# Kernel optimization log

Measured on AMD Instinct MI355X. Metric: run time of the kernel, lower is better.

The kernel has to match this reference:

```python
import jax, jax.numpy as jnp
import numpy as np
from jax import lax

# dims
B, T, D = 2, 1024, 512
H, K, V = 8, 64, 64      # head_k_dim = head_v_dim = 64
CONV = 4
# IVON / module hyperparams (from __init__ defaults)
LR, B1, B2, WD, LAM = 1e-3, 0.9, 0.999, 0.0, 1.0
EPS = 1e-5               # RMSNorm eps
SCALE = K ** -0.5


def _silu(x):
    return x * jax.nn.sigmoid(x)


def _short_conv(x, w):
    """Causal depthwise conv1d (kernel_size=CONV, no bias) + SiLU. x:[B,T,C], w:[C,CONV]."""
    xp = jnp.pad(x, ((0, 0), (CONV - 1, 0), (0, 0)))
    y = sum(xp[:, i:i + x.shape[1]] * w[:, i] for i in range(CONV))
    return _silu(y)


def _l2norm(x):
    return x * lax.rsqrt(jnp.sum(x * x, -1, keepdims=True) + 1e-6)


def setup_inputs() -> dict:
    key = jax.random.key(0)
    ks = jax.random.split(key, 10)
    s = 0.02
    return {
        "hidden_states": jax.random.normal(ks[0], (B, T, D), jnp.float32),
        "Wq": jax.random.normal(ks[1], (D, H * K), jnp.float32) * s,
        "Wk": jax.random.normal(ks[2], (D, H * K), jnp.float32) * s,
        "Wv": jax.random.normal(ks[3], (D, H * V), jnp.float32) * s,
        "Wb": jax.random.normal(ks[4], (D, H), jnp.float32) * s,
        "cw_q": jax.random.normal(ks[5], (H * K, CONV), jnp.float32) * 0.5,
        "cw_k": jax.random.normal(ks[6], (H * K, CONV), jnp.float32) * 0.5,
        "cw_v": jax.random.normal(ks[7], (H * V, CONV), jnp.float32) * 0.5,
        "rms_w": jnp.ones((V,), jnp.float32),
        "Wo": jax.random.normal(ks[8], (H * V, D), jnp.float32) * s,
    }


def reference(hidden_states, Wq, Wk, Wv, Wb, cw_q, cw_k, cw_v, rms_w, Wo):
    x = hidden_states
    # projections -> causal depthwise short conv (+SiLU, qk_activation='silu')
    q = _short_conv(x @ Wq, cw_q).reshape(B, T, H, K)
    k = _short_conv(x @ Wk, cw_k).reshape(B, T, H, K)
    v = _short_conv(x @ Wv, cw_v).reshape(B, T, H, V)
    beta = jax.nn.sigmoid(x @ Wb)                     # [B,T,H]
    # qk l2-norm inside kernel (qk_norm='l2'), scale on q
    q = _l2norm(q) * SCALE
    k = _l2norm(k)

    # fused recurrent IVON delta-rule: per-step outer-product gradient of
    # 0.5||k @ S - v||^2, momentum g, diag preconditioner h (noise-free IVON).
    def step(carry, inp):
        S, h, g = carry                               # each [B,H,K,V]
        qt, kt, vt, bt = inp                          # [B,H,K],[B,H,K],[B,H,V],[B,H]
        pred = jnp.einsum('bhk,bhkv->bhv', kt, S)
        grad = kt[..., None] * (pred - vt)[..., None, :]   # [B,H,K,V]
        g = B1 * g + (1.0 - B1) * grad
        h = B2 * h + (1.0 - B2) * grad * grad
        S = S - LR * bt[..., None, None] * (g + WD * S) / (h + LAM)
        o = jnp.einsum('bhk,bhkv->bhv', qt, S)
        return (S, h, g), o

    z = jnp.zeros((B, H, K, V), jnp.float32)
    inps = (jnp.swapaxes(q, 0, 1), jnp.swapaxes(k, 0, 1),
            jnp.swapaxes(v, 0, 1), jnp.swapaxes(beta, 0, 1))
    _, o = lax.scan(step, (z, z, z), inps)            # o: [T,B,H,V]
    o = jnp.swapaxes(o, 0, 1)                          # [B,T,H,V]

    # RMSNorm over head_v_dim, then output projection
    o = o * lax.rsqrt(jnp.mean(o * o, -1, keepdims=True) + EPS) * rms_w
    o = o.reshape(B, T, H * V) @ Wo                    # [B,T,D]
    return o
```

## Files before the change

### kernel.cpp

```cpp
#include <hip/hip_runtime.h>
#include <hip/hip_bf16.h>
#include <math.h>

#define Bb 2
#define Tt 1024
#define Dd 512
#define Hh 8
#define Kk 64
#define Vv 64
#define BT (Bb*Tt)
#define HK (Hh*Kk)

#define B1c 0.9f
#define B2c 0.999f
#define LRc 1e-3f
#define SCALEc 0.125f

typedef short s8v __attribute__((ext_vector_type(8)));
typedef float f4v __attribute__((ext_vector_type(4)));

__device__ __forceinline__ unsigned short f2bf(float x) {
  unsigned u = __float_as_uint(x);
  u += 0x7FFFu + ((u >> 16) & 1u);
  return (unsigned short)(u >> 16);
}
__device__ __forceinline__ float bf2f(unsigned short h) {
  return __uint_as_float((unsigned)h << 16);
}

template <int CTRL>
__device__ __forceinline__ float dpp_add(float v) {
  int y = __builtin_amdgcn_update_dpp(0, __float_as_int(v), CTRL, 0xF, 0xF, true);
  return v + __int_as_float(y);
}

typedef unsigned uint2_t __attribute__((ext_vector_type(2)));

__device__ __forceinline__ float xor16_add(float x) {
#if __has_builtin(__builtin_amdgcn_permlane16_swap)
  uint2_t r = __builtin_amdgcn_permlane16_swap(__float_as_uint(x), __float_as_uint(x),
                                               false, false);
  return __uint_as_float(r.x) + __uint_as_float(r.y);
#else
  int y = __builtin_amdgcn_ds_swizzle(__float_as_int(x), 0x401F);
  return x + __int_as_float(y);
#endif
}

__device__ __forceinline__ float xor32_add(float x) {
#if __has_builtin(__builtin_amdgcn_permlane32_swap)
  uint2_t r = __builtin_amdgcn_permlane32_swap(__float_as_uint(x), __float_as_uint(x),
                                               false, false);
  return __uint_as_float(r.x) + __uint_as_float(r.y);
#else
  return x + __shfl_xor(x, 32, 64);
#endif
}

__device__ __forceinline__ float reduce16(float x) {
  x = dpp_add<0xB1>(x);
  x = dpp_add<0x4E>(x);
  x = dpp_add<0x141>(x);
  x = dpp_add<0x140>(x);
  return x;
}

__device__ __forceinline__ float reduce64(float x) {
  x = reduce16(x);
  x = xor16_add(x);
  x = xor32_add(x);
  return x;
}

__global__ __launch_bounds__(256) void cvt_x_kernel(
    const float* __restrict__ x, unsigned short* __restrict__ hi,
    unsigned short* __restrict__ lo) {
  const int i = (blockIdx.x * 256 + threadIdx.x) * 8;
  float4 a = *(const float4*)(x + i);
  float4 b = *(const float4*)(x + i + 4);
  const float v[8] = {a.x, a.y, a.z, a.w, b.x, b.y, b.z, b.w};
  union { unsigned short u[8]; uint4 q; } ph, pl;
#pragma unroll
  for (int j = 0; j < 8; ++j) {
    unsigned short h = f2bf(v[j]);
    ph.u[j] = h;
    pl.u[j] = f2bf(v[j] - bf2f(h));
  }
  *(uint4*)(hi + i) = ph.q;
  *(uint4*)(lo + i) = pl.q;
}

__global__ __launch_bounds__(256) void cvt_w_kernel(
    const float* __restrict__ W0, const float* __restrict__ W1,
    const float* __restrict__ W2,
    unsigned short* __restrict__ hib, unsigned short* __restrict__ lob) {
  __shared__ float Ts[64][65];
  const int z = blockIdx.z;
  const float* W = (z == 0) ? W0 : (z == 1) ? W1 : W2;
  unsigned short* hi = hib + (size_t)z * 512 * 512;
  unsigned short* lo = lob + (size_t)z * 512 * 512;
  const int tk = blockIdx.x * 64;
  const int tn = blockIdx.y * 64;
  const int r  = threadIdx.x >> 2;
  const int cg = threadIdx.x & 3;
#pragma unroll
  for (int j = 0; j < 4; ++j) {
    float4 v = *(const float4*)(W + (size_t)(tk + r) * 512 + tn + cg * 16 + j * 4);
    Ts[r][cg * 16 + j * 4 + 0] = v.x;
    Ts[r][cg * 16 + j * 4 + 1] = v.y;
    Ts[r][cg * 16 + j * 4 + 2] = v.z;
    Ts[r][cg * 16 + j * 4 + 3] = v.w;
  }
  __syncthreads();
  union { unsigned short u[16]; uint4 q[2]; } ph, pl;
#pragma unroll
  for (int j = 0; j < 16; ++j) {
    float v = Ts[cg * 16 + j][r];
    unsigned short h = f2bf(v);
    ph.u[j] = h;
    pl.u[j] = f2bf(v - bf2f(h));
  }
  const size_t ob = (size_t)(tn + r) * 512 + tk + cg * 16;
  *(uint4*)(hi + ob) = ph.q[0];
  *(uint4*)(hi + ob + 8) = ph.q[1];
  *(uint4*)(lo + ob) = pl.q[0];
  *(uint4*)(lo + ob + 8) = pl.q[1];
}

__device__ __forceinline__ void gemm_mfma_body(
    const unsigned short* __restrict__ Ahi, const unsigned short* __restrict__ Alo,
    const unsigned short* __restrict__ Bhi, const unsigned short* __restrict__ Blo,
    float* __restrict__ C) {
  __shared__ unsigned short Ah[64][40], Al[64][40], Bh[64][40], Bl[64][40];
  const int tid = threadIdx.x;
  const int bm = blockIdx.x * 64;
  const int bn = blockIdx.y * 64;
  const int srow = tid >> 2;
  const int skoff = (tid & 3) * 8;
  const int l = tid & 63, w = tid >> 6;
  const int arow = (l & 15) + 16 * w;
  const int koff = (l >> 4) * 8;

  const unsigned short* pAh = Ahi + (size_t)(bm + srow) * 512 + skoff;
  const unsigned short* pAl = Alo + (size_t)(bm + srow) * 512 + skoff;
  const unsigned short* pBh = Bhi + (size_t)(bn + srow) * 512 + skoff;
  const unsigned short* pBl = Blo + (size_t)(bn + srow) * 512 + skoff;

  f4v acc0 = {0.f, 0.f, 0.f, 0.f}, acc1 = acc0, acc2 = acc0, acc3 = acc0;

  uint4 rah = *(const uint4*)(pAh);
  uint4 ral = *(const uint4*)(pAl);
  uint4 rbh = *(const uint4*)(pBh);
  uint4 rbl = *(const uint4*)(pBl);

  for (int k0 = 0; k0 < 512; k0 += 32) {
    __syncthreads();
    *(uint4*)&Ah[srow][skoff] = rah;
    *(uint4*)&Al[srow][skoff] = ral;
    *(uint4*)&Bh[srow][skoff] = rbh;
    *(uint4*)&Bl[srow][skoff] = rbl;
    __syncthreads();
    if (k0 + 32 < 512) {
      rah = *(const uint4*)(pAh + k0 + 32);
      ral = *(const uint4*)(pAl + k0 + 32);
      rbh = *(const uint4*)(pBh + k0 + 32);
      rbl = *(const uint4*)(pBl + k0 + 32);
    }
    const s8v ah = *(const s8v*)&Ah[arow][koff];
    const s8v al = *(const s8v*)&Al[arow][koff];
#pragma unroll
    for (int c = 0; c < 4; ++c) {
      const s8v bh = *(const s8v*)&Bh[16 * c + (l & 15)][koff];
      const s8v bl = *(const s8v*)&Bl[16 * c + (l & 15)][koff];
      f4v* acc = (c == 0) ? &acc0 : (c == 1) ? &acc1 : (c == 2) ? &acc2 : &acc3;
      *acc = __builtin_amdgcn_mfma_f32_16x16x32_bf16(al, bh, *acc, 0, 0, 0);
      *acc = __builtin_amdgcn_mfma_f32_16x16x32_bf16(ah, bl, *acc, 0, 0, 0);
      *acc = __builtin_amdgcn_mfma_f32_16x16x32_bf16(ah, bh, *acc, 0, 0, 0);
    }
  }

  const int crow = bm + 16 * w + (l >> 4) * 4;
  const int ccol = bn + (l & 15);
#pragma unroll
  for (int i = 0; i < 4; ++i) {
    C[(size_t)(crow + i) * 512 + ccol + 0]  = acc0[i];
    C[(size_t)(crow + i) * 512 + ccol + 16] = acc1[i];
    C[(size_t)(crow + i) * 512 + ccol + 32] = acc2[i];
    C[(size_t)(crow + i) * 512 + ccol + 48] = acc3[i];
  }
}

__global__ __launch_bounds__(256) void gemm3_mfma_kernel(
    const unsigned short* __restrict__ xhi, const unsigned short* __restrict__ xlo,
    const unsigned short* __restrict__ whi, const unsigned short* __restrict__ wlo,
    float* __restrict__ qp, float* __restrict__ kp, float* __restrict__ vp) {
  const int z = blockIdx.z;
  float* Cp = (z == 0) ? qp : (z == 1) ? kp : vp;
  gemm_mfma_body(xhi, xlo, whi + (size_t)z * 512 * 512, wlo + (size_t)z * 512 * 512, Cp);
}

__global__ __launch_bounds__(256) void gemm1_mfma_kernel(
    const unsigned short* __restrict__ ahi, const unsigned short* __restrict__ alo,
    const unsigned short* __restrict__ whi, const unsigned short* __restrict__ wlo,
    float* __restrict__ C) {
  gemm_mfma_body(ahi, alo, whi, wlo, C);
}

__global__ __launch_bounds__(256) void beta_kernel(const float* __restrict__ x,
                                                   const float* __restrict__ Wb,
                                                   float* __restrict__ beta) {
  int gid = blockIdx.x * blockDim.x + threadIdx.x;
  int bt = gid >> 3, h = gid & 7;
  const float4* xr = (const float4*)(x + (size_t)bt * Dd);
  float s = 0.f;
#pragma unroll 4
  for (int d4 = 0; d4 < Dd / 4; ++d4) {
    float4 xv = xr[d4];
    const float* wb = Wb + (d4 * 4) * Hh + h;
    s = fmaf(xv.x, wb[0 * Hh], s);
    s = fmaf(xv.y, wb[1 * Hh], s);
    s = fmaf(xv.z, wb[2 * Hh], s);
    s = fmaf(xv.w, wb[3 * Hh], s);
  }
  beta[gid] = 1.f / (1.f + expf(-s));
}

__global__ __launch_bounds__(256) void conv_kernel(
    const float* __restrict__ qp, const float* __restrict__ kp,
    const float* __restrict__ vp,
    const float* __restrict__ cwq, const float* __restrict__ cwk,
    const float* __restrict__ cwv,
    float* __restrict__ qc, float* __restrict__ kc, float* __restrict__ vc) {
  const int mode = blockIdx.z;
  const float* pre; const float* cw; float* post;
  if (mode == 0)      { pre = qp; cw = cwq; post = qc; }
  else if (mode == 1) { pre = kp; cw = cwk; post = kc; }
  else                { pre = vp; cw = cwv; post = vc; }

  const int idx = blockIdx.x * 4 + (threadIdx.x >> 6);
  const int lane = threadIdx.x & 63;
  const int b = idx >> 13;
  const int th = idx & 8191;
  const int t = th >> 3;
  const int h = th & 7;
  const int ch = h * 64 + lane;

  float y = 0.f;
#pragma unroll
  for (int i = 0; i < 4; ++i) {
    int tt = t + i - 3;
    if (tt >= 0)
      y += pre[((size_t)(b * Tt + tt)) * HK + ch] * cw[ch * 4 + i];
  }
  y = y / (1.f + expf(-y));
  if (mode < 2) {
    float ss = reduce64(y * y);
    y *= rsqrtf(ss + 1e-6f);
    if (mode == 0) y *= SCALEc;
  }
  post[((size_t)(b * Tt + t)) * HK + ch] = y;
}

#define TC 32
#define NT (Tt / TC)

__global__ __launch_bounds__(512) void scan_kernel(
    const float* __restrict__ qc, const float* __restrict__ kc,
    const float* __restrict__ vc, const float* __restrict__ beta,
    float* __restrict__ o) {
  __shared__ float  ks[3][TC][64];
  __shared__ float  qs[3][TC][64];
  __shared__ float2 vb[3][TC][4];
  __shared__ float  Sb[2][TC][4][64];

  const int tid  = threadIdx.x;
  const int lane = tid & 63;
  const int wave = tid >> 6;
  const int bid  = blockIdx.x;
  const int vq   = bid >> 4;
  const int bh   = bid & 15;
  const int b = bh >> 3, h = bh & 7;

  const size_t base2 = ((size_t)b * Tt) * HK + h * 64;
  const float* bp = beta + ((size_t)b * Tt) * Hh + h;

  const int tid2 = tid - 256;
  const int sr = (tid2 & 255) >> 4;
  const int sg = tid2 & 15;
  const int vr = (tid2 & 255) >> 3;
  const int vcc = tid2 & 3;

  if (wave >= 4) {
    float4 k0 = *(const float4*)(kc + base2 + (size_t)sr * HK + sg * 4);
    float4 q0 = *(const float4*)(qc + base2 + (size_t)sr * HK + sg * 4);
    float4 k1 = *(const float4*)(kc + base2 + (size_t)(sr + 16) * HK + sg * 4);
    float4 q1 = *(const float4*)(qc + base2 + (size_t)(sr + 16) * HK + sg * 4);
    *(float4*)&ks[0][sr][sg * 4] = k0;
    *(float4*)&qs[0][sr][sg * 4] = q0;
    *(float4*)&ks[0][sr + 16][sg * 4] = k1;
    *(float4*)&qs[0][sr + 16][sg * 4] = q1;
    if ((tid2 & 7) < 4) {
      float vv = vc[base2 + (size_t)vr * HK + vq * 4 + vcc];
      float lb = (0.1f * LRc) * bp[(size_t)vr * Hh];
      vb[0][vr][vcc] = make_float2(vv, lb);
    }
  }
  __syncthreads();

  float S = 0.f, G = 0.f, H = 0.f, r = 1.f;
  float pred = 0.f;

  int d = 0;
  for (int tile = 0; tile < NT; ++tile) {
    const int dn = (d + 1 == 3) ? 0 : d + 1;
    const int dm = (d == 0) ? 2 : d - 1;
    const int sb = tile & 1, sbp = sb ^ 1;
    const int t0 = tile * TC;
    const int more = (tile + 1 < NT);

    if (wave < 4) {
      const int w = wave;
      pred = reduce64(ks[d][0][lane] * S);
#pragma unroll
      for (int s = 0; s < TC; ++s) {
        const float kv = ks[d][s][lane];
        const float2 vbc = vb[d][s][w];
        const float diff = pred - vbc.x;
        const float lrb = vbc.y;
        const float gr = kv * diff;
        G = fmaf(B1c, G, gr);
        H = fmaf(B2c, H, gr * gr);
        const float dd = fmaf(H, 0.001f, 1.0f);
        r = r * fmaf(-dd, r, 2.0f);
        S = fmaf(-lrb, G * r, S);
        Sb[sb][s][w][lane] = S;
        if (s + 1 < TC)
          pred = reduce64(ks[d][s + 1][lane] * S);
      }
    } else {
      float4 nk0, nq0, nk1, nq1; float nv = 0.f, nb = 0.f;
      if (more) {
        const int tn = t0 + TC;
        nk0 = *(const float4*)(kc + base2 + (size_t)(tn + sr) * HK + sg * 4);
        nq0 = *(const float4*)(qc + base2 + (size_t)(tn + sr) * HK + sg * 4);
        nk1 = *(const float4*)(kc + base2 + (size_t)(tn + sr + 16) * HK + sg * 4);
        nq1 = *(const float4*)(qc + base2 + (size_t)(tn + sr + 16) * HK + sg * 4);
        if ((tid2 & 7) < 4) {
          nv = vc[base2 + (size_t)(tn + vr) * HK + vq * 4 + vcc];
          nb = (0.1f * LRc) * bp[(size_t)(tn + vr) * Hh];
        }
      }
      if (tile > 0) {
        const int cb = wave - 4;
        float* opc = o + base2 + vq * 4 + cb;
        const int tp0 = t0 - TC;
#pragma unroll
        for (int s = 0; s < TC; ++s) {
          const float qv = qs[dm][s][lane];
          const float Sv = Sb[sbp][s][cb][lane];
          const float po = reduce64(qv * Sv);
          opc[(size_t)(tp0 + s) * HK] = po;
        }
      }
      if (more) {
        *(float4*)&ks[dn][sr][sg * 4] = nk0;
        *(float4*)&qs[dn][sr][sg * 4] = nq0;
        *(float4*)&ks[dn][sr + 16][sg * 4] = nk1;
        *(float4*)&qs[dn][sr + 16][sg * 4] = nq1;
        if ((tid2 & 7) < 4) vb[dn][vr][vcc] = make_float2(nv, nb);
      }
    }
    __syncthreads();
    d = dn;
  }

  if (wave >= 4) {
    const int dlast = (NT - 1) % 3;
    const int sbl = (NT - 1) & 1;
    const int cb = wave - 4;
    float* opc = o + base2 + vq * 4 + cb;
    const int tp0 = (NT - 1) * TC;
#pragma unroll
    for (int s = 0; s < TC; ++s) {
      const float qv = qs[dlast][s][lane];
      const float Sv = Sb[sbl][s][cb][lane];
      const float po = reduce64(qv * Sv);
      opc[(size_t)(tp0 + s) * HK] = po;
    }
  }
}

__global__ __launch_bounds__(256) void rmsnorm_kernel(
    const float* __restrict__ o, const float* __restrict__ rmsw,
    unsigned short* __restrict__ hi, unsigned short* __restrict__ lo) {
  const int idx = blockIdx.x * 4 + (threadIdx.x >> 6);
  const int lane = threadIdx.x & 63;
  const float* p = o + (size_t)idx * 64;
  float y = p[lane];
  float ss = reduce64(y * y);
  y = y * rsqrtf(ss * (1.f / 64.f) + 1e-5f) * rmsw[lane];
  unsigned short h = f2bf(y);
  hi[(size_t)idx * 64 + lane] = h;
  lo[(size_t)idx * 64 + lane] = f2bf(y - bf2f(h));
}

extern "C" void kernel_launch(void* const* d_in, const int* in_sizes, int n_in,
                              void* d_out, int out_size, void* d_ws, size_t ws_size,
                              hipStream_t stream) {
  const float* x    = (const float*)d_in[0];
  const float* Wq   = (const float*)d_in[1];
  const float* Wk   = (const float*)d_in[2];
  const float* Wv   = (const float*)d_in[3];
  const float* Wb   = (const float*)d_in[4];
  const float* cwq  = (const float*)d_in[5];
  const float* cwk  = (const float*)d_in[6];
  const float* cwv  = (const float*)d_in[7];
  const float* rmsw = (const float*)d_in[8];
  const float* Wo   = (const float*)d_in[9];
  float* out = (float*)d_out;
  float* ws  = (float*)d_ws;

  const size_t SZ = (size_t)BT * HK;
  float* qp   = ws;
  float* kp   = ws + 1 * SZ;
  float* vp   = ws + 2 * SZ;
  float* qc   = ws + 3 * SZ;
  float* kc   = ws + 4 * SZ;
  float* vc   = ws + 5 * SZ;
  float* beta = ws + 6 * SZ;
  float* on   = qp;

  unsigned short* xhi  = (unsigned short*)qc;
  unsigned short* xlo  = xhi + SZ;
  unsigned short* wh3  = (unsigned short*)kc;
  unsigned short* wl3  = wh3 + 3 * 512 * 512;
  unsigned short* wohi = (unsigned short*)vc;
  unsigned short* wolo = wohi + 512 * 512;
  unsigned short* onhi = (unsigned short*)kp;
  unsigned short* onlo = (unsigned short*)vp;

  cvt_x_kernel<<<dim3(BT * Dd / (256 * 8)), 256, 0, stream>>>(x, xhi, xlo);
  cvt_w_kernel<<<dim3(8, 8, 3), 256, 0, stream>>>(Wq, Wk, Wv, wh3, wl3);
  gemm3_mfma_kernel<<<dim3(BT / 64, HK / 64, 3), 256, 0, stream>>>(
      xhi, xlo, wh3, wl3, qp, kp, vp);
  beta_kernel<<<dim3(BT * Hh / 256), 256, 0, stream>>>(x, Wb, beta);
  conv_kernel<<<dim3(Bb * Tt * Hh / 4, 1, 3), 256, 0, stream>>>(
      qp, kp, vp, cwq, cwk, cwv, qc, kc, vc);
  scan_kernel<<<dim3(Bb * Hh * (Vv / 4)), 512, 0, stream>>>(
      qc, kc, vc, beta, on);
  cvt_w_kernel<<<dim3(8, 8, 1), 256, 0, stream>>>(Wo, Wo, Wo, wohi, wolo);
  rmsnorm_kernel<<<dim3(Bb * Tt * Hh / 4), 256, 0, stream>>>(on, rmsw, onhi, onlo);
  gemm1_mfma_kernel<<<dim3(BT / 64, HK / 64, 1), 256, 0, stream>>>(
      onhi, onlo, wohi, wolo, out);
}
```

Measured before the change: 180.4 us.

## Pack scan state into one compute wave with 4 K-rows per lane

The recurrent scan now runs in a single wave instead of four. Each lane holds four K entries of the state, and 16 lanes cover one V column, so each step's prediction needs a 16-lane reduction rather than a 64-lane one. The goal is to shorten the serial per-timestep reduction chain and add instruction-level parallelism on the critical path. The block shrinks to 320 threads, with four loader/output waves kept as before. The trade-off is more registers per lane and more per-step arithmetic serialized within that one wave.

```diff
diff --git a/kernel.cpp b/kernel.cpp
--- a/kernel.cpp
+++ b/kernel.cpp
@@ -264,7 +264,7 @@
 #define TC 32
 #define NT (Tt / TC)
 
-__global__ __launch_bounds__(512) void scan_kernel(
+__global__ __launch_bounds__(320) void scan_kernel(
     const float* __restrict__ qc, const float* __restrict__ kc,
     const float* __restrict__ vc, const float* __restrict__ beta,
     float* __restrict__ o) {
@@ -284,13 +284,16 @@
   const size_t base2 = ((size_t)b * Tt) * HK + h * 64;
   const float* bp = beta + ((size_t)b * Tt) * Hh + h;
 
-  const int tid2 = tid - 256;
+  const int g    = lane & 15;
+  const int cgrp = lane >> 4;
+
+  const int tid2 = tid - 64;
   const int sr = (tid2 & 255) >> 4;
   const int sg = tid2 & 15;
   const int vr = (tid2 & 255) >> 3;
   const int vcc = tid2 & 3;
 
-  if (wave >= 4) {
+  if (wave >= 1) {
     float4 k0 = *(const float4*)(kc + base2 + (size_t)sr * HK + sg * 4);
     float4 q0 = *(const float4*)(qc + base2 + (size_t)sr * HK + sg * 4);
     float4 k1 = *(const float4*)(kc + base2 + (size_t)(sr + 16) * HK + sg * 4);
@@ -307,8 +310,10 @@
   }
   __syncthreads();
 
-  float S = 0.f, G = 0.f, H = 0.f, r = 1.f;
-  float pred = 0.f;
+  float S0 = 0, S1 = 0, S2 = 0, S3 = 0;
+  float G0 = 0, G1 = 0, G2 = 0, G3 = 0;
+  float H0 = 0, H1 = 0, H2 = 0, H3 = 0;
+  float r0 = 1.f, r1 = 1.f, r2 = 1.f, r3 = 1.f;
 
   int d = 0;
   for (int tile = 0; tile < NT; ++tile) {
@@ -318,24 +323,46 @@
     const int t0 = tile * TC;
     const int more = (tile + 1 < NT);
 
-    if (wave < 4) {
-      const int w = wave;
-      pred = reduce64(ks[d][0][lane] * S);
+    if (wave == 0) {
+      float4 kt = *(const float4*)&ks[d][0][g * 4];
+      float pred = reduce16(fmaf(kt.x, S0, kt.y * S1) +
+                            fmaf(kt.z, S2, kt.w * S3));
 #pragma unroll
       for (int s = 0; s < TC; ++s) {
-        const float kv = ks[d][s][lane];
-        const float2 vbc = vb[d][s][w];
+        const float4 kv = *(const float4*)&ks[d][s][g * 4];
+        const float2 vbc = vb[d][s][cgrp];
         const float diff = pred - vbc.x;
         const float lrb = vbc.y;
-        const float gr = kv * diff;
-        G = fmaf(B1c, G, gr);
-        H = fmaf(B2c, H, gr * gr);
-        const float dd = fmaf(H, 0.001f, 1.0f);
-        r = r * fmaf(-dd, r, 2.0f);
-        S = fmaf(-lrb, G * r, S);
-        Sb[sb][s][w][lane] = S;
-        if (s + 1 < TC)
-          pred = reduce64(ks[d][s + 1][lane] * S);
+        const float gr0 = kv.x * diff;
+        const float gr1 = kv.y * diff;
+        const float gr2 = kv.z * diff;
+        const float gr3 = kv.w * diff;
+        G0 = fmaf(B1c, G0, gr0);
+        G1 = fmaf(B1c, G1, gr1);
+        G2 = fmaf(B1c, G2, gr2);
+        G3 = fmaf(B1c, G3, gr3);
+        H0 = fmaf(B2c, H0, gr0 * gr0);
+        H1 = fmaf(B2c, H1, gr1 * gr1);
+        H2 = fmaf(B2c, H2, gr2 * gr2);
+        H3 = fmaf(B2c, H3, gr3 * gr3);
+        const float d0 = fmaf(H0, 0.001f, 1.0f);
+        const float d1 = fmaf(H1, 0.001f, 1.0f);
+        const float d2 = fmaf(H2, 0.001f, 1.0f);
+        const float d3 = fmaf(H3, 0.001f, 1.0f);
+        r0 = r0 * fmaf(-d0, r0, 2.0f);
+        r1 = r1 * fmaf(-d1, r1, 2.0f);
+        r2 = r2 * fmaf(-d2, r2, 2.0f);
+        r3 = r3 * fmaf(-d3, r3, 2.0f);
+        S0 = fmaf(-lrb, G0 * r0, S0);
+        S1 = fmaf(-lrb, G1 * r1, S1);
+        S2 = fmaf(-lrb, G2 * r2, S2);
+        S3 = fmaf(-lrb, G3 * r3, S3);
+        *(float4*)&Sb[sb][s][cgrp][g * 4] = make_float4(S0, S1, S2, S3);
+        if (s + 1 < TC) {
+          const float4 k1 = *(const float4*)&ks[d][s + 1][g * 4];
+          pred = reduce16(fmaf(k1.x, S0, k1.y * S1) +
+                          fmaf(k1.z, S2, k1.w * S3));
+        }
       }
     } else {
       float4 nk0, nq0, nk1, nq1; float nv = 0.f, nb = 0.f;
@@ -351,7 +378,7 @@
         }
       }
       if (tile > 0) {
-        const int cb = wave - 4;
+        const int cb = wave - 1;
         float* opc = o + base2 + vq * 4 + cb;
         const int tp0 = t0 - TC;
 #pragma unroll
@@ -374,10 +401,10 @@
     d = dn;
   }
 
-  if (wave >= 4) {
+  if (wave >= 1) {
     const int dlast = (NT - 1) % 3;
     const int sbl = (NT - 1) & 1;
-    const int cb = wave - 4;
+    const int cb = wave - 1;
     float* opc = o + base2 + vq * 4 + cb;
     const int tp0 = (NT - 1) * TC;
 #pragma unroll
@@ -446,7 +473,7 @@
   beta_kernel<<<dim3(BT * Hh / 256), 256, 0, stream>>>(x, Wb, beta);
   conv_kernel<<<dim3(Bb * Tt * Hh / 4, 1, 3), 256, 0, stream>>>(
       qp, kp, vp, cwq, cwk, cwv, qc, kc, vc);
-  scan_kernel<<<dim3(Bb * Hh * (Vv / 4)), 512, 0, stream>>>(
+  scan_kernel<<<dim3(Bb * Hh * (Vv / 4)), 320, 0, stream>>>(
       qc, kc, vc, beta, on);
   cvt_w_kernel<<<dim3(8, 8, 1), 256, 0, stream>>>(Wo, Wo, Wo, wohi, wolo);
   rmsnorm_kernel<<<dim3(Bb * Tt * Hh / 4), 256, 0, stream>>>(on, rmsw, onhi, onlo);
```

New measurement: 195.4 us. 8.3% more time.
